# Performance work log

Hardware: AMD Instinct MI355X
Metric: run time of the kernel (lower is better)

## Reference

```python
import jax, jax.numpy as jnp
import numpy as np

S, L, K = 4, 256, 32          # num_states, seq length, neighbors
ORIG_H, EMB_H, EXV, RANK = 128, 256, 384, 16


def _integrate(x, Wq, Wk, seq_idx, emb_idx, hidden, rank):
    """AttentionIntegrator.forward: QK^T softmax -> double mean -> softmax -> weighted pool of raw x."""
    x = jnp.moveaxis(x, (seq_idx, emb_idx), (-2, -1))
    orig_shape = x.shape
    Ls = orig_shape[-2]
    xf = x.reshape(-1, Ls, hidden)               # (B, Ls, hidden)
    B = xf.shape[0]
    q = (xf @ Wq.T).reshape(B, Ls, rank, hidden)  # head_dim == hidden
    k = (xf @ Wk.T).reshape(B, Ls, rank, hidden)
    scale = 1.0 / jnp.sqrt(jnp.asarray(hidden, xf.dtype))
    scores = jnp.einsum('blhd,bmhd->bhlm', q, k) * scale
    attn = jax.nn.softmax(scores, axis=-1)        # (B, rank, Ls, Ls)
    w = jax.nn.softmax(attn.mean(axis=(1, 2)), axis=-1)  # (B, Ls)
    pooled = jnp.einsum('bl,bld->bd', w, xf)      # (B, hidden)
    return (pooled.reshape(*orig_shape[:-2], hidden),
            w.reshape(*orig_shape[:-2], Ls))


def setup_inputs() -> dict:
    key = jax.random.key(0)
    ks = jax.random.split(key, 12)
    sc = lambda fan_in: 1.0 / np.sqrt(fan_in)
    return {
        'h_V':    jax.random.normal(ks[0], (S, L, ORIG_H), jnp.float32),
        'h_EXV':  jax.random.normal(ks[1], (S, L, K, EXV), jnp.float32),
        'W_hV':   jax.random.normal(ks[2], (EMB_H, ORIG_H), jnp.float32) * sc(ORIG_H),
        'b_hV':   jnp.zeros((EMB_H,), jnp.float32),
        'Wq_hv':  jax.random.normal(ks[3], (RANK * EMB_H, EMB_H), jnp.float32) * sc(EMB_H),
        'Wk_hv':  jax.random.normal(ks[4], (RANK * EMB_H, EMB_H), jnp.float32) * sc(EMB_H),
        'Wq_ce':  jax.random.normal(ks[5], (RANK * EXV, EXV), jnp.float32) * sc(EXV),
        'Wk_ce':  jax.random.normal(ks[6], (RANK * EXV, EXV), jnp.float32) * sc(EXV),
        'W_ce':   jax.random.normal(ks[7], (EMB_H, EXV), jnp.float32) * sc(EXV),
        'b_ce':   jnp.zeros((EMB_H,), jnp.float32),
        'Wq_sce': jax.random.normal(ks[8], (RANK * EMB_H, EMB_H), jnp.float32) * sc(EMB_H),
        'Wk_sce': jax.random.normal(ks[9], (RANK * EMB_H, EMB_H), jnp.float32) * sc(EMB_H),
    }


def reference(h_V, h_EXV, W_hV, b_hV, Wq_hv, Wk_hv, Wq_ce, Wk_ce, W_ce, b_ce, Wq_sce, Wk_sce):
    # diffmodel.get_weights
    hv = h_V @ W_hV.T + b_hV                                  # (S, L, EMB_H)
    h_V_int, h_V_w = _integrate(hv, Wq_hv, Wk_hv, 0, 2, EMB_H, RANK)   # pool over states
    # chemical environment: pool over k neighbors per (state, position)
    ce, _local_w = _integrate(h_EXV, Wq_ce, Wk_ce, 2, 3, EXV, RANK)    # (S, L, EXV)
    ce = ce @ W_ce.T + b_ce                                   # (S, L, EMB_H)
    ce_int, ce_w = _integrate(ce, Wq_sce, Wk_sce, 0, 2, EMB_H, RANK)   # pool over states
    return (h_V_int[None], h_V_w[None], ce_int[None], ce_w[None])
```

## Files before the change

kernel.cpp:

```cpp
#include <hip/hip_runtime.h>

typedef _Float16 f16;
typedef _Float16 f16x8 __attribute__((ext_vector_type(8)));
typedef float f32x4 __attribute__((ext_vector_type(4)));

#define MFMA16(a, b, c) __builtin_amdgcn_mfma_f32_16x16x32_f16(a, b, c, 0, 0, 0)

__global__ __launch_bounds__(256) void k_mt(const float* __restrict__ Wq,
                                            const float* __restrict__ Wk,
                                            f16* __restrict__ MT, int H) {
    const int h = blockIdx.x;
    const int ntile = H >> 6;
    const int nkk = H >> 5;
    const int frow = (blockIdx.y / ntile) * 64;
    const int ecol = (blockIdx.y % ntile) * 64;
    const int t = threadIdx.x;
    const int lane = t & 63;
    const int w = t >> 6;
    const int wr = w >> 1, wc = w & 1;

    __shared__ __align__(16) f16 As[64][40];
    __shared__ __align__(16) f16 Ks[64][40];

    f32x4 acc[2][2] = {};
    const int d = t >> 3;
    const int e8 = (t & 7) * 8;

    for (int kk = 0; kk < nkk; ++kk) {
        const float* gq = Wq + (size_t)(h * H + kk * 32 + d) * H + ecol + e8;
        const float* gk = Wk + (size_t)(h * H + kk * 32 + d) * H + frow + e8;
        float q[8], k[8];
#pragma unroll
        for (int i = 0; i < 8; ++i) { q[i] = gq[i]; k[i] = gk[i]; }
        __syncthreads();
#pragma unroll
        for (int i = 0; i < 8; ++i) { As[e8 + i][d] = (f16)q[i]; Ks[e8 + i][d] = (f16)k[i]; }
        __syncthreads();
        f16x8 a[2], b[2];
#pragma unroll
        for (int rt = 0; rt < 2; ++rt)
            a[rt] = *(const f16x8*)&Ks[wr * 32 + rt * 16 + (lane & 15)][(lane >> 4) * 8];
#pragma unroll
        for (int nt = 0; nt < 2; ++nt)
            b[nt] = *(const f16x8*)&As[wc * 32 + nt * 16 + (lane & 15)][(lane >> 4) * 8];
#pragma unroll
        for (int rt = 0; rt < 2; ++rt)
#pragma unroll
            for (int nt = 0; nt < 2; ++nt)
                acc[rt][nt] = MFMA16(a[rt], b[nt], acc[rt][nt]);
    }
#pragma unroll
    for (int rt = 0; rt < 2; ++rt)
#pragma unroll
        for (int nt = 0; nt < 2; ++nt)
#pragma unroll
            for (int j = 0; j < 4; ++j) {
                int f = frow + wr * 32 + rt * 16 + (lane >> 4) * 4 + j;
                int e = ecol + wc * 32 + nt * 16 + (lane & 15);
                MT[(((size_t)h * nkk + (e >> 5)) * H + f) * 32 + (e & 31)] = (f16)acc[rt][nt][j];
            }
}

__global__ __launch_bounds__(256) void k_lin(const float* __restrict__ in,
                                             const float* __restrict__ W,
                                             const float* __restrict__ bias,
                                             float* __restrict__ out, int K) {
    const int t = threadIdx.x;
    const int r0 = blockIdx.x * 4;
    __shared__ float ins[4][384];
    __shared__ float Ws[256][33];
#pragma unroll
    for (int r = 0; r < 4; ++r)
        for (int off = t; off < K; off += 256)
            ins[r][off] = in[(size_t)(r0 + r) * K + off];
    float acc[4] = {};
    for (int d0 = 0; d0 < K; d0 += 32) {
        __syncthreads();
        for (int i = t; i < 256 * 32; i += 256) {
            int j = i >> 5, dd = i & 31;
            Ws[j][dd] = W[(size_t)j * K + d0 + dd];
        }
        __syncthreads();
#pragma unroll 8
        for (int dd = 0; dd < 32; ++dd) {
            float wv = Ws[t][dd];
#pragma unroll
            for (int r = 0; r < 4; ++r) acc[r] += wv * ins[r][d0 + dd];
        }
    }
    float bv = bias[t];
#pragma unroll
    for (int r = 0; r < 4; ++r) out[(size_t)(r0 + r) * 256 + t] = acc[r] + bv;
}

__global__ __launch_bounds__(256) void k_small_int(const float* __restrict__ X,
                                                   const f16* __restrict__ MT,
                                                   float* __restrict__ wpart) {
    const int t = threadIdx.x;
    const int lane = t & 63;
    const int w = t >> 6;
    const int g = lane >> 4;
    const int l15 = lane & 15;
    const int pos0 = blockIdx.x * 16;
    const int h = blockIdx.y;

    extern __shared__ __align__(16) char smem0[];
    f16(*Xs)[264] = (f16(*)[264])smem0;
    f16(*Ts)[264] = (f16(*)[264])(smem0 + 33792);

    {
        int row = t >> 2, d0 = (t & 3) * 64;
        int s = row & 3, p = row >> 2;
        const float* gx = X + (size_t)(s * 256 + pos0 + p) * 256 + d0;
#pragma unroll
        for (int i = 0; i < 8; ++i) {
            float4 v0 = *(const float4*)(gx + i * 8);
            float4 v1 = *(const float4*)(gx + i * 8 + 4);
            f16x8 o;
            o[0] = (f16)v0.x; o[1] = (f16)v0.y; o[2] = (f16)v0.z; o[3] = (f16)v0.w;
            o[4] = (f16)v1.x; o[5] = (f16)v1.y; o[6] = (f16)v1.z; o[7] = (f16)v1.w;
            *(f16x8*)&Xs[row][d0 + i * 8] = o;
        }
    }
    __syncthreads();

    const f16* mh = MT + (size_t)h * 8 * 256 * 32;
    const int fb = w * 64 + l15;
    f32x4 acc[4][4] = {};
    f16x8 bq[4], bn[4];
#pragma unroll
    for (int nt = 0; nt < 4; ++nt)
        bq[nt] = *(const f16x8*)(mh + (size_t)(fb + nt * 16) * 32 + g * 8);
#pragma unroll
    for (int kk = 0; kk < 8; ++kk) {
        if (kk < 7) {
#pragma unroll
            for (int nt = 0; nt < 4; ++nt)
                bn[nt] = *(const f16x8*)(mh + ((size_t)(kk + 1) * 256 + fb + nt * 16) * 32 + g * 8);
        }
        f16x8 a[4];
#pragma unroll
        for (int rt = 0; rt < 4; ++rt)
            a[rt] = *(const f16x8*)&Xs[rt * 16 + l15][kk * 32 + g * 8];
#pragma unroll
        for (int rt = 0; rt < 4; ++rt)
#pragma unroll
            for (int nt = 0; nt < 4; ++nt)
                acc[rt][nt] = MFMA16(a[rt], bq[nt], acc[rt][nt]);
#pragma unroll
        for (int nt = 0; nt < 4; ++nt) bq[nt] = bn[nt];
    }
#pragma unroll
    for (int rt = 0; rt < 4; ++rt)
#pragma unroll
        for (int nt = 0; nt < 4; ++nt)
#pragma unroll
            for (int j = 0; j < 4; ++j)
                Ts[rt * 16 + g * 4 + j][w * 64 + nt * 16 + l15] = (f16)acc[rt][nt][j];
    __syncthreads();

    f32x4 sacc = {};
#pragma unroll
    for (int ks = 0; ks < 8; ++ks) {
        f16x8 a = *(const f16x8*)&Ts[w * 16 + l15][ks * 32 + g * 8];
        f16x8 b = *(const f16x8*)&Xs[w * 16 + l15][ks * 32 + g * 8];
        sacc = MFMA16(a, b, sacc);
    }
    if ((l15 >> 2) == g) {
        const float scale = 1.0f / 16.0f;
        float add = 0.f;
#pragma unroll
        for (int j = 0; j < 4; ++j) {
            float v = sacc[j] * scale;
            float m = v;
            m = fmaxf(m, __shfl_xor(m, 1));
            m = fmaxf(m, __shfl_xor(m, 2));
            float e = expf(v - m);
            float s2 = e;
            s2 += __shfl_xor(s2, 1);
            s2 += __shfl_xor(s2, 2);
            add += e / s2;
        }
        int pg = pos0 + w * 4 + g;
        wpart[((size_t)h * 256 + pg) * 4 + (l15 & 3)] = add;
    }
}

__global__ __launch_bounds__(256) void k_small_fin(const float* __restrict__ wpart,
                                                   const float* __restrict__ X,
                                                   float* __restrict__ out_int,
                                                   float* __restrict__ out_w) {
    const int pos = blockIdx.x, t = threadIdx.x;
    __shared__ float red[64];
    __shared__ float ws[4];
    if (t < 64) red[t] = wpart[((size_t)(t >> 2) * 256 + pos) * 4 + (t & 3)];
    __syncthreads();
    if (t == 0) {
        float v[4];
#pragma unroll
        for (int s = 0; s < 4; ++s) {
            float x = 0.f;
            for (int hh = 0; hh < 16; ++hh) x += red[hh * 4 + s];
            v[s] = x * (1.0f / 64.0f);
        }
        float m = fmaxf(fmaxf(v[0], v[1]), fmaxf(v[2], v[3]));
        float sum = 0.f;
#pragma unroll
        for (int s = 0; s < 4; ++s) { v[s] = expf(v[s] - m); sum += v[s]; }
#pragma unroll
        for (int s = 0; s < 4; ++s) ws[s] = v[s] / sum;
    }
    __syncthreads();
    if (t < 4) out_w[pos * 4 + t] = ws[t];
    float v = 0.f;
#pragma unroll
    for (int s = 0; s < 4; ++s) v += ws[s] * X[(size_t)(s * 256 + pos) * 256 + t];
    out_int[(size_t)pos * 256 + t] = v;
}

#define TS_OFF 49152
#define AP_OFF 66560

__global__ __launch_bounds__(256, 2) void k_ce_int(const float* __restrict__ Xg32,
                                                   const f16* __restrict__ MT,
                                                   float* __restrict__ acc_out) {
    const int t = threadIdx.x;
    const int lane = t & 63;
    const int w = t >> 6;
    const int g = lane >> 4;
    const int l15 = lane & 15;
    const int bg = blockIdx.x;

    extern __shared__ __align__(16) char smem[];
    float* ap = (float*)(smem + AP_OFF);

    {
        const float* xg = Xg32 + (size_t)bg * 64 * 384;
#pragma unroll
        for (int p = 0; p < 12; ++p) {
            int idx = p * 256 + t;
            int row = idx / 48, s = idx - row * 48;
            int c = s ^ (row & 7);
            const float* src = xg + row * 384 + c * 8;
            float4 v0 = *(const float4*)src;
            float4 v1 = *(const float4*)(src + 4);
            f16x8 o;
            o[0] = (f16)v0.x; o[1] = (f16)v0.y; o[2] = (f16)v0.z; o[3] = (f16)v0.w;
            o[4] = (f16)v1.x; o[5] = (f16)v1.y; o[6] = (f16)v1.z; o[7] = (f16)v1.w;
            *(f16x8*)(smem + idx * 16) = o;
        }
    }
    __syncthreads();

    for (int hi = 0; hi < 4; ++hi) {
        const int h = blockIdx.y * 4 + hi;
        const f16* mh = MT + (size_t)h * 12 * 384 * 32;

        f32x4 acc[4][6] = {};
        f16x8 bq[6], bn[6];
#pragma unroll
        for (int nt = 0; nt < 6; ++nt)
            bq[nt] = *(const f16x8*)(mh + (size_t)(w * 96 + nt * 16 + l15) * 32 + g * 8);
#pragma unroll
        for (int kk = 0; kk < 12; ++kk) {
            if (kk < 11) {
#pragma unroll
                for (int nt = 0; nt < 6; ++nt)
                    bn[nt] = *(const f16x8*)(mh + ((size_t)(kk + 1) * 384 + w * 96 + nt * 16 + l15) * 32 + g * 8);
            }
            f16x8 a[4];
#pragma unroll
            for (int rt = 0; rt < 4; ++rt) {
                int row = rt * 16 + l15;
                int ch = kk * 4 + g;
                a[rt] = *(const f16x8*)(smem + row * 768 + ((ch ^ (row & 7)) << 4));
            }
#pragma unroll
            for (int rt = 0; rt < 4; ++rt)
#pragma unroll
                for (int nt = 0; nt < 6; ++nt)
                    acc[rt][nt] = MFMA16(a[rt], bq[nt], acc[rt][nt]);
#pragma unroll
            for (int nt = 0; nt < 6; ++nt) bq[nt] = bn[nt];
        }

        const int b = w >> 1, lt = w & 1;
        f32x4 s2[2] = {};
#pragma unroll
        for (int c = 0; c < 3; ++c) {
#pragma unroll
            for (int nt = 0; nt < 6; ++nt) {
                int col0 = w * 96 + nt * 16;
                if ((col0 >> 7) == c) {
#pragma unroll
                    for (int rt = 0; rt < 4; ++rt)
#pragma unroll
                        for (int j = 0; j < 4; ++j) {
                            int l = rt * 16 + g * 4 + j;
                            int cl = col0 + l15 - c * 128;
                            *(f16*)(smem + TS_OFF + l * 272 + cl * 2) = (f16)acc[rt][nt][j];
                        }
                }
            }
            __syncthreads();
#pragma unroll
            for (int ks = 0; ks < 4; ++ks) {
                int l = b * 32 + lt * 16 + l15;
                f16x8 a2 = *(const f16x8*)(smem + TS_OFF + l * 272 + (ks * 32 + g * 8) * 2);
#pragma unroll
                for (int nt2 = 0; nt2 < 2; ++nt2) {
                    int m = b * 32 + nt2 * 16 + l15;
                    int ch = c * 16 + ks * 4 + g;
                    f16x8 b2 = *(const f16x8*)(smem + m * 768 + ((ch ^ (m & 7)) << 4));
                    s2[nt2] = MFMA16(a2, b2, s2[nt2]);
                }
            }
            __syncthreads();
        }

        const float scale = 0.051031036307982884f;
        float cp0 = 0.f, cp1 = 0.f;
#pragma unroll
        for (int j = 0; j < 4; ++j) {
            float v0 = s2[0][j] * scale, v1 = s2[1][j] * scale;
            float m = fmaxf(v0, v1);
            m = fmaxf(m, __shfl_xor(m, 1));
            m = fmaxf(m, __shfl_xor(m, 2));
            m = fmaxf(m, __shfl_xor(m, 4));
            m = fmaxf(m, __shfl_xor(m, 8));
            float e0 = expf(v0 - m), e1 = expf(v1 - m);
            float s = e0 + e1;
            s += __shfl_xor(s, 1);
            s += __shfl_xor(s, 2);
            s += __shfl_xor(s, 4);
            s += __shfl_xor(s, 8);
            float inv = 1.f / s;
            cp0 += e0 * inv;
            cp1 += e1 * inv;
        }
        cp0 += __shfl_xor(cp0, 16); cp0 += __shfl_xor(cp0, 32);
        cp1 += __shfl_xor(cp1, 16); cp1 += __shfl_xor(cp1, 32);
        if (lane < 16) {
            ap[w * 32 + lane] = cp0;
            ap[w * 32 + 16 + lane] = cp1;
        }
        __syncthreads();
        if (t < 64) {
            int bb = t >> 5, m = t & 31;
            float v = ap[bb * 64 + m] + ap[bb * 64 + 32 + m];
            acc_out[((size_t)h * 1024 + bg * 2 + bb) * 32 + m] = v;
        }
        __syncthreads();
    }
}

__global__ __launch_bounds__(128) void k_ce_pool(const float* __restrict__ accp,
                                                 const float* __restrict__ exv,
                                                 float* __restrict__ pooled) {
    const int b = blockIdx.x;
    const int t = threadIdx.x;
    __shared__ float wm[32];
    __shared__ float ww[32];
    if (t < 32) {
        float s = 0.f;
#pragma unroll
        for (int h = 0; h < 16; ++h) s += accp[((size_t)h * 1024 + b) * 32 + t];
        wm[t] = s * (1.0f / 512.0f);
    }
    __syncthreads();
    if (t == 0) {
        float m = wm[0];
        for (int i = 1; i < 32; ++i) m = fmaxf(m, wm[i]);
        float s = 0.f;
        for (int i = 0; i < 32; ++i) { float e = expf(wm[i] - m); ww[i] = e; s += e; }
        float inv = 1.f / s;
        for (int i = 0; i < 32; ++i) ww[i] *= inv;
    }
    __syncthreads();
    for (int d = t; d < 384; d += 128) {
        float v = 0.f;
#pragma unroll
        for (int m = 0; m < 32; ++m) v += ww[m] * exv[((size_t)b * 32 + m) * 384 + d];
        pooled[(size_t)b * 384 + d] = v;
    }
}

extern "C" void kernel_launch(void* const* d_in, const int* in_sizes, int n_in,
                              void* d_out, int out_size, void* d_ws, size_t ws_size,
                              hipStream_t stream) {
    const float* h_V    = (const float*)d_in[0];
    const float* h_EXV  = (const float*)d_in[1];
    const float* W_hV   = (const float*)d_in[2];
    const float* b_hV   = (const float*)d_in[3];
    const float* Wq_hv  = (const float*)d_in[4];
    const float* Wk_hv  = (const float*)d_in[5];
    const float* Wq_ce  = (const float*)d_in[6];
    const float* Wk_ce  = (const float*)d_in[7];
    const float* W_ce   = (const float*)d_in[8];
    const float* b_ce   = (const float*)d_in[9];
    const float* Wq_sce = (const float*)d_in[10];
    const float* Wk_sce = (const float*)d_in[11];
    float* out = (float*)d_out;

    char* ws = (char*)d_ws;
    f16*   mt_hv  = (f16*)(ws + 0);
    f16*   mt_sce = (f16*)(ws + 2097152);
    f16*   mt_ce  = (f16*)(ws + 4194304);
    float* hv     = (float*)(ws + 8912896);
    float* ce     = (float*)(ws + 9961472);
    float* accp   = (float*)(ws + 11010048);
    float* pooled = (float*)(ws + 13107200);
    float* wpart  = accp;

    k_mt<<<dim3(16, 16), 256, 0, stream>>>(Wq_hv, Wk_hv, mt_hv, 256);
    k_mt<<<dim3(16, 36), 256, 0, stream>>>(Wq_ce, Wk_ce, mt_ce, 384);
    k_mt<<<dim3(16, 16), 256, 0, stream>>>(Wq_sce, Wk_sce, mt_sce, 256);
    k_lin<<<256, 256, 0, stream>>>(h_V, W_hV, b_hV, hv, 128);
    k_small_int<<<dim3(16, 16), 256, 67584, stream>>>(hv, mt_hv, wpart);
    k_small_fin<<<256, 256, 0, stream>>>(wpart, hv, out + 0, out + 65536);
    k_ce_int<<<dim3(512, 4), 256, 67072, stream>>>(h_EXV, mt_ce, accp);
    k_ce_pool<<<1024, 128, 0, stream>>>(accp, h_EXV, pooled);
    k_lin<<<256, 256, 0, stream>>>(pooled, W_ce, b_ce, ce, 384);
    k_small_int<<<dim3(16, 16), 256, 67584, stream>>>(ce, mt_sce, wpart);
    k_small_fin<<<256, 256, 0, stream>>>(wpart, ce, out + 66560, out + 132096);
}
```

Measured before the change: 349.0 us.

## Restructure ce attention kernel: all heads per block, register-resident second GEMM

The chemical-environment integrator kernel now processes all 16 rank heads in one block, so the 64x384 input tile is loaded and converted to fp16 once instead of four times. The first GEMM is transposed so its accumulators can be converted to fp16 and fed directly as operands to 16x16x16 MFMAs for the QK^T scores. This removes the shared-memory staging of the projected tile and two barriers per chunk. Partial score sums from the four waves are reduced through shared memory, and the softmax column sums are written per query-half, so the pool kernel now reads twice as many partials. The grid shrinks from 2048 to 512 blocks, which may hurt latency hiding and occupancy in exchange for less redundant loading and fewer syncs.

```diff
diff --git a/kernel.cpp b/kernel.cpp
--- a/kernel.cpp
+++ b/kernel.cpp
@@ -2,9 +2,11 @@
 
 typedef _Float16 f16;
 typedef _Float16 f16x8 __attribute__((ext_vector_type(8)));
+typedef _Float16 f16x4 __attribute__((ext_vector_type(4)));
 typedef float f32x4 __attribute__((ext_vector_type(4)));
 
 #define MFMA16(a, b, c) __builtin_amdgcn_mfma_f32_16x16x32_f16(a, b, c, 0, 0, 0)
+#define MFMA16K16(a, b, c) __builtin_amdgcn_mfma_f32_16x16x16f16(a, b, c, 0, 0, 0)
 
 __global__ __launch_bounds__(256) void k_mt(const float* __restrict__ Wq,
                                             const float* __restrict__ Wk,
@@ -218,8 +220,7 @@
     out_int[(size_t)pos * 256 + t] = v;
 }
 
-#define TS_OFF 49152
-#define AP_OFF 66560
+#define PART_OFF 49152
 
 __global__ __launch_bounds__(256, 2) void k_ce_int(const float* __restrict__ Xg32,
                                                    const f16* __restrict__ MT,
@@ -232,7 +233,6 @@
     const int bg = blockIdx.x;
 
     extern __shared__ __align__(16) char smem[];
-    float* ap = (float*)(smem + AP_OFF);
 
     {
         const float* xg = Xg32 + (size_t)bg * 64 * 384;
@@ -252,103 +252,135 @@
     }
     __syncthreads();
 
-    for (int hi = 0; hi < 4; ++hi) {
-        const int h = blockIdx.y * 4 + hi;
-        const f16* mh = MT + (size_t)h * 12 * 384 * 32;
-
-        f32x4 acc[4][6] = {};
-        f16x8 bq[6], bn[6];
-#pragma unroll
-        for (int nt = 0; nt < 6; ++nt)
-            bq[nt] = *(const f16x8*)(mh + (size_t)(w * 96 + nt * 16 + l15) * 32 + g * 8);
+    const f16* mall = MT;
+    const int frow = w * 96 + l15;
+
+    f16x8 aq[6], an[6];
+#pragma unroll
+    for (int ft = 0; ft < 6; ++ft)
+        aq[ft] = *(const f16x8*)(mall + ((size_t)0 * 384 + frow + ft * 16) * 32 + g * 8);
+
+    for (int hi = 0; hi < 16; ++hi) {
+        f32x4 acc[6][4] = {};
 #pragma unroll
         for (int kk = 0; kk < 12; ++kk) {
-            if (kk < 11) {
-#pragma unroll
-                for (int nt = 0; nt < 6; ++nt)
-                    bn[nt] = *(const f16x8*)(mh + ((size_t)(kk + 1) * 384 + w * 96 + nt * 16 + l15) * 32 + g * 8);
-            }
-            f16x8 a[4];
-#pragma unroll
-            for (int rt = 0; rt < 4; ++rt) {
-                int row = rt * 16 + l15;
+            int nstep = hi * 12 + kk + 1;
+            if (nstep < 192) {
+#pragma unroll
+                for (int ft = 0; ft < 6; ++ft)
+                    an[ft] = *(const f16x8*)(mall + ((size_t)nstep * 384 + frow + ft * 16) * 32 + g * 8);
+            }
+            f16x8 xb[4];
+#pragma unroll
+            for (int mt = 0; mt < 4; ++mt) {
+                int row = mt * 16 + l15;
                 int ch = kk * 4 + g;
-                a[rt] = *(const f16x8*)(smem + row * 768 + ((ch ^ (row & 7)) << 4));
-            }
-#pragma unroll
-            for (int rt = 0; rt < 4; ++rt)
-#pragma unroll
-                for (int nt = 0; nt < 6; ++nt)
-                    acc[rt][nt] = MFMA16(a[rt], bq[nt], acc[rt][nt]);
-#pragma unroll
-            for (int nt = 0; nt < 6; ++nt) bq[nt] = bn[nt];
-        }
-
-        const int b = w >> 1, lt = w & 1;
-        f32x4 s2[2] = {};
-#pragma unroll
-        for (int c = 0; c < 3; ++c) {
-#pragma unroll
-            for (int nt = 0; nt < 6; ++nt) {
-                int col0 = w * 96 + nt * 16;
-                if ((col0 >> 7) == c) {
-#pragma unroll
-                    for (int rt = 0; rt < 4; ++rt)
-#pragma unroll
-                        for (int j = 0; j < 4; ++j) {
-                            int l = rt * 16 + g * 4 + j;
-                            int cl = col0 + l15 - c * 128;
-                            *(f16*)(smem + TS_OFF + l * 272 + cl * 2) = (f16)acc[rt][nt][j];
-                        }
+                xb[mt] = *(const f16x8*)(smem + row * 768 + ((ch ^ (row & 7)) << 4));
+            }
+#pragma unroll
+            for (int ft = 0; ft < 6; ++ft)
+#pragma unroll
+                for (int mt = 0; mt < 4; ++mt)
+                    acc[ft][mt] = MFMA16(aq[ft], xb[mt], acc[ft][mt]);
+#pragma unroll
+            for (int ft = 0; ft < 6; ++ft) aq[ft] = an[ft];
+        }
+
+        f16x4 bf[6][4];
+#pragma unroll
+        for (int ft = 0; ft < 6; ++ft)
+#pragma unroll
+            for (int mt = 0; mt < 4; ++mt) {
+                f32x4 v = acc[ft][mt];
+                f16x4 o;
+                o[0] = (f16)v[0]; o[1] = (f16)v[1]; o[2] = (f16)v[2]; o[3] = (f16)v[3];
+                bf[ft][mt] = o;
+            }
+
+        f32x4 s2[2][2][2] = {};
+#pragma unroll
+        for (int b = 0; b < 2; ++b)
+#pragma unroll
+            for (int ks = 0; ks < 6; ++ks)
+#pragma unroll
+                for (int it = 0; it < 2; ++it) {
+                    int r = b * 32 + it * 16 + l15;
+                    int ch = 12 * w + 2 * ks + (g >> 1);
+                    f16x4 av = *(const f16x4*)(smem + r * 768 + ((ch ^ (r & 7)) << 4) + 8 * (g & 1));
+#pragma unroll
+                    for (int lt = 0; lt < 2; ++lt)
+                        s2[b][it][lt] = MFMA16K16(av, bf[ks][2 * b + lt], s2[b][it][lt]);
                 }
-            }
-            __syncthreads();
-#pragma unroll
-            for (int ks = 0; ks < 4; ++ks) {
-                int l = b * 32 + lt * 16 + l15;
-                f16x8 a2 = *(const f16x8*)(smem + TS_OFF + l * 272 + (ks * 32 + g * 8) * 2);
-#pragma unroll
-                for (int nt2 = 0; nt2 < 2; ++nt2) {
-                    int m = b * 32 + nt2 * 16 + l15;
-                    int ch = c * 16 + ks * 4 + g;
-                    f16x8 b2 = *(const f16x8*)(smem + m * 768 + ((ch ^ (m & 7)) << 4));
-                    s2[nt2] = MFMA16(a2, b2, s2[nt2]);
+
+#pragma unroll
+        for (int b = 0; b < 2; ++b)
+#pragma unroll
+            for (int lt = 0; lt < 2; ++lt) {
+                int dst = b * 2 + lt;
+                if (dst != w) {
+                    int src = w - (w > dst ? 1 : 0);
+#pragma unroll
+                    for (int it = 0; it < 2; ++it)
+                        *(f32x4*)(smem + PART_OFF + (((dst * 3 + src) * 2 + it) << 10) + lane * 16) =
+                            s2[b][it][lt];
                 }
             }
-            __syncthreads();
-        }
-
-        const float scale = 0.051031036307982884f;
-        float cp0 = 0.f, cp1 = 0.f;
-#pragma unroll
-        for (int j = 0; j < 4; ++j) {
-            float v0 = s2[0][j] * scale, v1 = s2[1][j] * scale;
-            float m = fmaxf(v0, v1);
-            m = fmaxf(m, __shfl_xor(m, 1));
-            m = fmaxf(m, __shfl_xor(m, 2));
-            m = fmaxf(m, __shfl_xor(m, 4));
-            m = fmaxf(m, __shfl_xor(m, 8));
-            float e0 = expf(v0 - m), e1 = expf(v1 - m);
-            float s = e0 + e1;
-            s += __shfl_xor(s, 1);
-            s += __shfl_xor(s, 2);
-            s += __shfl_xor(s, 4);
-            s += __shfl_xor(s, 8);
-            float inv = 1.f / s;
-            cp0 += e0 * inv;
-            cp1 += e1 * inv;
-        }
-        cp0 += __shfl_xor(cp0, 16); cp0 += __shfl_xor(cp0, 32);
-        cp1 += __shfl_xor(cp1, 16); cp1 += __shfl_xor(cp1, 32);
-        if (lane < 16) {
-            ap[w * 32 + lane] = cp0;
-            ap[w * 32 + 16 + lane] = cp1;
-        }
-        __syncthreads();
-        if (t < 64) {
-            int bb = t >> 5, m = t & 31;
-            float v = ap[bb * 64 + m] + ap[bb * 64 + 32 + m];
-            acc_out[((size_t)h * 1024 + bg * 2 + bb) * 32 + m] = v;
+        __syncthreads();
+
+        {
+            const int b = w >> 1, lt = w & 1;
+            f32x4 own0, own1;
+            if (w == 0)      { own0 = s2[0][0][0]; own1 = s2[0][1][0]; }
+            else if (w == 1) { own0 = s2[0][0][1]; own1 = s2[0][1][1]; }
+            else if (w == 2) { own0 = s2[1][0][0]; own1 = s2[1][1][0]; }
+            else             { own0 = s2[1][0][1]; own1 = s2[1][1][1]; }
+            f32x4 ssum[2] = { own0, own1 };
+#pragma unroll
+            for (int src = 0; src < 3; ++src)
+#pragma unroll
+                for (int it = 0; it < 2; ++it)
+                    ssum[it] += *(const f32x4*)(smem + PART_OFF + (((w * 3 + src) * 2 + it) << 10) + lane * 16);
+
+            const float scale = 0.051031036307982884f;
+            float mx = -1e30f;
+#pragma unroll
+            for (int it = 0; it < 2; ++it)
+#pragma unroll
+                for (int j = 0; j < 4; ++j) mx = fmaxf(mx, ssum[it][j] * scale);
+            mx = fmaxf(mx, __shfl_xor(mx, 16));
+            mx = fmaxf(mx, __shfl_xor(mx, 32));
+            float e[2][4];
+            float den = 0.f;
+#pragma unroll
+            for (int it = 0; it < 2; ++it)
+#pragma unroll
+                for (int j = 0; j < 4; ++j) {
+                    e[it][j] = expf(ssum[it][j] * scale - mx);
+                    den += e[it][j];
+                }
+            den += __shfl_xor(den, 16);
+            den += __shfl_xor(den, 32);
+            float inv = 1.f / den;
+            float cs[2][4];
+#pragma unroll
+            for (int it = 0; it < 2; ++it)
+#pragma unroll
+                for (int j = 0; j < 4; ++j) {
+                    float v = e[it][j] * inv;
+                    v += __shfl_xor(v, 1);
+                    v += __shfl_xor(v, 2);
+                    v += __shfl_xor(v, 4);
+                    v += __shfl_xor(v, 8);
+                    cs[it][j] = v;
+                }
+            if (l15 == 0) {
+                float* o = acc_out + (((size_t)hi * 1024 + bg * 2 + b) * 2 + lt) * 32;
+#pragma unroll
+                for (int it = 0; it < 2; ++it)
+#pragma unroll
+                    for (int j = 0; j < 4; ++j)
+                        o[it * 16 + g * 4 + j] = cs[it][j];
+            }
         }
         __syncthreads();
     }
@@ -364,7 +396,10 @@
     if (t < 32) {
         float s = 0.f;
 #pragma unroll
-        for (int h = 0; h < 16; ++h) s += accp[((size_t)h * 1024 + b) * 32 + t];
+        for (int h = 0; h < 16; ++h) {
+            s += accp[(((size_t)h * 1024 + b) * 2 + 0) * 32 + t];
+            s += accp[(((size_t)h * 1024 + b) * 2 + 1) * 32 + t];
+        }
         wm[t] = s * (1.0f / 512.0f);
     }
     __syncthreads();
@@ -409,7 +444,7 @@
     float* hv     = (float*)(ws + 8912896);
     float* ce     = (float*)(ws + 9961472);
     float* accp   = (float*)(ws + 11010048);
-    float* pooled = (float*)(ws + 13107200);
+    float* pooled = (float*)(ws + 15204352);
     float* wpart  = accp;
 
     k_mt<<<dim3(16, 16), 256, 0, stream>>>(Wq_hv, Wk_hv, mt_hv, 256);
@@ -418,7 +453,7 @@
     k_lin<<<256, 256, 0, stream>>>(h_V, W_hV, b_hV, hv, 128);
     k_small_int<<<dim3(16, 16), 256, 67584, stream>>>(hv, mt_hv, wpart);
     k_small_fin<<<256, 256, 0, stream>>>(wpart, hv, out + 0, out + 65536);
-    k_ce_int<<<dim3(512, 4), 256, 67072, stream>>>(h_EXV, mt_ce, accp);
+    k_ce_int<<<dim3(512), 256, 73728, stream>>>(h_EXV, mt_ce, accp);
     k_ce_pool<<<1024, 128, 0, stream>>>(accp, h_EXV, pooled);
     k_lin<<<256, 256, 0, stream>>>(pooled, W_ce, b_ce, ce, 384);
     k_small_int<<<dim3(16, 16), 256, 67584, stream>>>(ce, mt_sce, wpart);
```

Result: faster. 328.9 us (-5.8%).
